# Kernel optimization log

Measured on AMD Instinct MI355X. Metric: run time of the kernel, lower is better.

The kernel has to match this reference:

```python
import jax, jax.numpy as jnp
import numpy as np

SHIFT = 1  # shift_direction fixed to +1 (original picks +/-1 randomly at init)


def setup_inputs() -> dict:
    key = jax.random.key(0)
    kx, kw = jax.random.split(key)
    x = jax.random.normal(kx, (128, 128, 56, 56), dtype=jnp.float32)  # (N, C, H, W)
    w = jax.random.normal(kw, (32, 3, 128), dtype=jnp.float32)        # (out_ch, ktap, in_ch)
    return {"x": x, "w": w}


def reference(x, w):
    # roll along W (original dim 3), then 1x3 conv along W with SAME padding,
    # then roll the output along H (original dim 2).
    xr = jnp.roll(x, SHIFT, axis=3)
    # einsum 'nkmilo,jki->njmlo' == correlation: y[n,j,h,w] = sum_{k,i} xr[n,i,h,w+k-1] * w[j,k,i]
    kernel = jnp.transpose(w, (0, 2, 1))[:, :, None, :]  # (O=32, I=128, kh=1, kw=3)
    y = jax.lax.conv_general_dilated(
        xr, kernel,
        window_strides=(1, 1),
        padding=((0, 0), (1, 1)),
        dimension_numbers=("NCHW", "OIHW", "NCHW"),
    )  # (128, 32, 56, 56)
    return jnp.roll(y, SHIFT, axis=2)
```

## Files before the change

### kernel.cpp

```cpp
#include <hip/hip_runtime.h>
#include <stddef.h>


#define C_IN   128
#define C_OUT  32
#define HH     56
#define WW     56
#define HW     3136
#define KTOT   384
#define WSTRIDE 392
#define XSTRIDE 136
#define XROW   (57 * XSTRIDE)

typedef short bf16x8 __attribute__((ext_vector_type(8)));
typedef float f32x4  __attribute__((ext_vector_type(4)));

static __device__ __forceinline__ unsigned short f2b(float f) {
    unsigned u = __builtin_bit_cast(unsigned, f);
    unsigned r = u + 0x7FFFu + ((u >> 16) & 1u);
    return (unsigned short)(r >> 16);
}

__global__ void pack_w_kernel(const float* __restrict__ w, unsigned short* __restrict__ ws) {
    int idx = blockIdx.x * 256 + threadIdx.x;
    if (idx < C_OUT * WSTRIDE) {
        int j = idx / WSTRIDE;
        int r = idx % WSTRIDE;
        ws[idx] = f2b(r < KTOT ? w[j * KTOT + r] : 0.0f);
    }
}

__global__ __launch_bounds__(256, 5)
void conv_mfma_kernel(const float* __restrict__ x, const unsigned short* __restrict__ ws,
                      float* __restrict__ out) {
    const int bid  = blockIdx.x;
    const int n    = bid / (HH / 2);
    const int h0   = (bid % (HH / 2)) * 2;
    const int tid  = threadIdx.x;
    const int lane = tid & 63;
    const int grp  = tid >> 6;

    __shared__ __align__(16) unsigned short XT[2 * XROW];

    if (tid < 32) {
        int r = tid >> 4, seg = tid & 15;
        *(uint4*)&XT[r * XROW + WW * XSTRIDE + seg * 8] = make_uint4(0, 0, 0, 0);
    }

    const int hp0 = (h0 + HH - 1) % HH;
    const float* xb = x + (size_t)n * (C_IN * HW);

#pragma unroll
    for (int p = 0; p < 14; ++p) {
        const int task = p * 256 + tid;
        const int ch   = task & 127;
        const int rest = task >> 7;
        const int c4   = rest % 14;
        const int r    = rest / 14;
        const int hrow = (r == 0) ? hp0 : h0;
        const float4 v = *(const float4*)(xb + (size_t)ch * HW + hrow * WW + c4 * 4);
        unsigned short* dst = &XT[r * XROW + (c4 * 4) * XSTRIDE + ch];
        dst[0]           = f2b(v.x);
        dst[XSTRIDE]     = f2b(v.y);
        dst[2 * XSTRIDE] = f2b(v.z);
        dst[3 * XSTRIDE] = f2b(v.w);
    }
    __syncthreads();

    const int nn = grp * 16 + (lane & 15);
    const int kb = (lane >> 4) * 8;
    const int cc0 = (nn >= 1 && nn <= 55) ? (nn + 54) % WW : WW;
    const int cc1 = (nn <= 55) ? (nn + 55) % WW : WW;
    const int cc2 = (nn <= 54) ? nn : WW;
    const unsigned short* b00 = &XT[cc0 * XSTRIDE + kb];
    const unsigned short* b01 = &XT[cc1 * XSTRIDE + kb];
    const unsigned short* b02 = &XT[cc2 * XSTRIDE + kb];

    const unsigned short* wp = ws + (lane & 15) * WSTRIDE + kb;

    f32x4 acc00 = {0.f,0.f,0.f,0.f}, acc01 = {0.f,0.f,0.f,0.f};
    f32x4 acc10 = {0.f,0.f,0.f,0.f}, acc11 = {0.f,0.f,0.f,0.f};

#pragma unroll
    for (int c = 0; c < 12; ++c) {
        const int tap = c >> 2;
        const int ib  = (c & 3) * 32;
        const unsigned short* bp = (tap == 0) ? b00 : (tap == 1) ? b01 : b02;
        bf16x8 A0 = *(const bf16x8*)(wp + c * 32);
        bf16x8 A1 = *(const bf16x8*)(wp + 16 * WSTRIDE + c * 32);
        bf16x8 B0 = *(const bf16x8*)(bp + ib);
        bf16x8 B1 = *(const bf16x8*)(bp + XROW + ib);
        acc00 = __builtin_amdgcn_mfma_f32_16x16x32_bf16(A0, B0, acc00, 0, 0, 0);
        acc01 = __builtin_amdgcn_mfma_f32_16x16x32_bf16(A1, B0, acc01, 0, 0, 0);
        acc10 = __builtin_amdgcn_mfma_f32_16x16x32_bf16(A0, B1, acc10, 0, 0, 0);
        acc11 = __builtin_amdgcn_mfma_f32_16x16x32_bf16(A1, B1, acc11, 0, 0, 0);
    }

    if (nn < WW) {
        const int j0 = (lane >> 4) * 4;
        float* ob = out + (size_t)n * (C_OUT * HW) + (size_t)h0 * WW + nn;
#pragma unroll
        for (int r = 0; r < 4; ++r) {
            ob[(size_t)(j0 + r) * HW]           = acc00[r];
            ob[(size_t)(j0 + r + 16) * HW]      = acc01[r];
            ob[(size_t)(j0 + r) * HW + WW]      = acc10[r];
            ob[(size_t)(j0 + r + 16) * HW + WW] = acc11[r];
        }
    }
}

extern "C" void kernel_launch(void* const* d_in, const int* in_sizes, int n_in,
                              void* d_out, int out_size, void* d_ws, size_t ws_size,
                              hipStream_t stream) {
    const float* x = (const float*)d_in[0];
    const float* w = (const float*)d_in[1];
    float* out = (float*)d_out;
    unsigned short* ws = (unsigned short*)d_ws;

    pack_w_kernel<<<(C_OUT * WSTRIDE + 255) / 256, 256, 0, stream>>>(w, ws);
    conv_mfma_kernel<<<dim3(128 * (HH / 2)), dim3(256), 0, stream>>>(x, ws, out);
}
```

Baseline: 322.5 us.

## Process four output rows per block with one wave per row

Result: faster. 303.5 us (-5.9%).

```diff
diff --git a/kernel.cpp b/kernel.cpp
--- a/kernel.cpp
+++ b/kernel.cpp
@@ -10,7 +10,7 @@
 #define KTOT   384
 #define WSTRIDE 392
 #define XSTRIDE 136
-#define XROW   (57 * XSTRIDE)
+#define XROWSZ (57 * XSTRIDE)
 
 typedef short bf16x8 __attribute__((ext_vector_type(8)));
 typedef float f32x4  __attribute__((ext_vector_type(4)));
@@ -30,81 +30,100 @@
     }
 }
 
-__global__ __launch_bounds__(256, 5)
+__global__ __launch_bounds__(256, 2)
 void conv_mfma_kernel(const float* __restrict__ x, const unsigned short* __restrict__ ws,
                       float* __restrict__ out) {
     const int bid  = blockIdx.x;
-    const int n    = bid / (HH / 2);
-    const int h0   = (bid % (HH / 2)) * 2;
+    const int n    = bid / (HH / 4);
+    const int h0   = (bid % (HH / 4)) * 4;
     const int tid  = threadIdx.x;
     const int lane = tid & 63;
     const int grp  = tid >> 6;
 
-    __shared__ __align__(16) unsigned short XT[2 * XROW];
+    __shared__ __align__(16) unsigned short XT[4 * XROWSZ];
 
-    if (tid < 32) {
-        int r = tid >> 4, seg = tid & 15;
-        *(uint4*)&XT[r * XROW + WW * XSTRIDE + seg * 8] = make_uint4(0, 0, 0, 0);
+    if (tid < 68) {
+        int r = tid / 17, off = (tid % 17) * 8;
+        *(uint4*)&XT[r * XROWSZ + WW * XSTRIDE + off] = make_uint4(0, 0, 0, 0);
     }
 
-    const int hp0 = (h0 + HH - 1) % HH;
     const float* xb = x + (size_t)n * (C_IN * HW);
 
-#pragma unroll
-    for (int p = 0; p < 14; ++p) {
-        const int task = p * 256 + tid;
-        const int ch   = task & 127;
-        const int rest = task >> 7;
-        const int c4   = rest % 14;
-        const int r    = rest / 14;
-        const int hrow = (r == 0) ? hp0 : h0;
-        const float4 v = *(const float4*)(xb + (size_t)ch * HW + hrow * WW + c4 * 4);
-        unsigned short* dst = &XT[r * XROW + (c4 * 4) * XSTRIDE + ch];
-        dst[0]           = f2b(v.x);
-        dst[XSTRIDE]     = f2b(v.y);
-        dst[2 * XSTRIDE] = f2b(v.z);
-        dst[3 * XSTRIDE] = f2b(v.w);
+    {
+        const int q  = lane;
+        const int r  = q / 14;
+        const int c4 = q % 14;
+        const int hs = (h0 + 55 + r) % HH;
+        const size_t rowoff = (size_t)hs * WW + c4 * 4;
+        unsigned short* dst0 = &XT[r * XROWSZ + (c4 * 4) * XSTRIDE];
+#pragma unroll 8
+        for (int p = 0; p < 32; ++p) {
+            const int ch = p * 4 + grp;
+            if (q < WW) {
+                const float4 v = *(const float4*)(xb + (size_t)ch * HW + rowoff);
+                unsigned short* dst = dst0 + ch;
+                dst[0]           = f2b(v.x);
+                dst[XSTRIDE]     = f2b(v.y);
+                dst[2 * XSTRIDE] = f2b(v.z);
+                dst[3 * XSTRIDE] = f2b(v.w);
+            }
+        }
     }
     __syncthreads();
 
-    const int nn = grp * 16 + (lane & 15);
-    const int kb = (lane >> 4) * 8;
-    const int cc0 = (nn >= 1 && nn <= 55) ? (nn + 54) % WW : WW;
-    const int cc1 = (nn <= 55) ? (nn + 55) % WW : WW;
-    const int cc2 = (nn <= 54) ? nn : WW;
-    const unsigned short* b00 = &XT[cc0 * XSTRIDE + kb];
-    const unsigned short* b01 = &XT[cc1 * XSTRIDE + kb];
-    const unsigned short* b02 = &XT[cc2 * XSTRIDE + kb];
+    const int l15 = lane & 15;
+    const int kb  = (lane >> 4) * 8;
+    const unsigned short* Xr = &XT[grp * XROWSZ];
 
-    const unsigned short* wp = ws + (lane & 15) * WSTRIDE + kb;
+    const unsigned short* bp[4][3];
+#pragma unroll
+    for (int ct = 0; ct < 4; ++ct) {
+        const int nn = ct * 16 + l15;
+        const int cc0 = (nn >= 1 && nn <= 55) ? (nn + 54) % WW : WW;
+        const int cc1 = (nn <= 55) ? (nn + 55) % WW : WW;
+        const int cc2 = (nn <= 54) ? nn : WW;
+        bp[ct][0] = Xr + cc0 * XSTRIDE + kb;
+        bp[ct][1] = Xr + cc1 * XSTRIDE + kb;
+        bp[ct][2] = Xr + cc2 * XSTRIDE + kb;
+    }
 
-    f32x4 acc00 = {0.f,0.f,0.f,0.f}, acc01 = {0.f,0.f,0.f,0.f};
-    f32x4 acc10 = {0.f,0.f,0.f,0.f}, acc11 = {0.f,0.f,0.f,0.f};
+    const unsigned short* wp = ws + l15 * WSTRIDE + kb;
+
+    f32x4 acc[4][2];
+#pragma unroll
+    for (int ct = 0; ct < 4; ++ct) {
+        acc[ct][0] = (f32x4){0.f, 0.f, 0.f, 0.f};
+        acc[ct][1] = (f32x4){0.f, 0.f, 0.f, 0.f};
+    }
 
 #pragma unroll
     for (int c = 0; c < 12; ++c) {
         const int tap = c >> 2;
         const int ib  = (c & 3) * 32;
-        const unsigned short* bp = (tap == 0) ? b00 : (tap == 1) ? b01 : b02;
         bf16x8 A0 = *(const bf16x8*)(wp + c * 32);
         bf16x8 A1 = *(const bf16x8*)(wp + 16 * WSTRIDE + c * 32);
-        bf16x8 B0 = *(const bf16x8*)(bp + ib);
-        bf16x8 B1 = *(const bf16x8*)(bp + XROW + ib);
-        acc00 = __builtin_amdgcn_mfma_f32_16x16x32_bf16(A0, B0, acc00, 0, 0, 0);
-        acc01 = __builtin_amdgcn_mfma_f32_16x16x32_bf16(A1, B0, acc01, 0, 0, 0);
-        acc10 = __builtin_amdgcn_mfma_f32_16x16x32_bf16(A0, B1, acc10, 0, 0, 0);
-        acc11 = __builtin_amdgcn_mfma_f32_16x16x32_bf16(A1, B1, acc11, 0, 0, 0);
+#pragma unroll
+        for (int ct = 0; ct < 4; ++ct) {
+            bf16x8 B = *(const bf16x8*)(bp[ct][tap] + ib);
+            acc[ct][0] = __builtin_amdgcn_mfma_f32_16x16x32_bf16(A0, B, acc[ct][0], 0, 0, 0);
+            acc[ct][1] = __builtin_amdgcn_mfma_f32_16x16x32_bf16(A1, B, acc[ct][1], 0, 0, 0);
+        }
     }
 
-    if (nn < WW) {
+    {
+        const int h  = h0 + grp;
         const int j0 = (lane >> 4) * 4;
-        float* ob = out + (size_t)n * (C_OUT * HW) + (size_t)h0 * WW + nn;
+        float* ob = out + (size_t)n * (C_OUT * HW) + (size_t)h * WW;
 #pragma unroll
-        for (int r = 0; r < 4; ++r) {
-            ob[(size_t)(j0 + r) * HW]           = acc00[r];
-            ob[(size_t)(j0 + r + 16) * HW]      = acc01[r];
-            ob[(size_t)(j0 + r) * HW + WW]      = acc10[r];
-            ob[(size_t)(j0 + r + 16) * HW + WW] = acc11[r];
+        for (int ct = 0; ct < 4; ++ct) {
+            const int nn = ct * 16 + l15;
+            if (nn < WW) {
+#pragma unroll
+                for (int r = 0; r < 4; ++r) {
+                    ob[(size_t)(j0 + r) * HW + nn]      = acc[ct][0][r];
+                    ob[(size_t)(j0 + r + 16) * HW + nn] = acc[ct][1][r];
+                }
+            }
         }
     }
 }
@@ -118,5 +137,5 @@
     unsigned short* ws = (unsigned short*)d_ws;
 
     pack_w_kernel<<<(C_OUT * WSTRIDE + 255) / 256, 256, 0, stream>>>(w, ws);
-    conv_mfma_kernel<<<dim3(128 * (HH / 2)), dim3(256), 0, stream>>>(x, ws, out);
+    conv_mfma_kernel<<<dim3(128 * (HH / 4)), dim3(256), 0, stream>>>(x, ws, out);
 }
```
